# Kernel optimization log

Measured on AMD Instinct MI355X. Metric: run time of the kernel, lower is better.

The kernel has to match this reference:

```python
import jax, jax.numpy as jnp
import numpy as np

D_MODEL = 1024
D_FF = 2048
N_EXPERTS = 8
TOP_K = 2


def setup_inputs() -> dict:
    key = jax.random.key(0)
    ks = jax.random.split(key, 10)
    s = 0.02
    return {
        "x": jax.random.normal(ks[0], (2, 1024, D_MODEL), dtype=jnp.float32),
        "gate_w": jax.random.normal(ks[1], (N_EXPERTS, D_MODEL), dtype=jnp.float32) * s,
        "gate_b": jnp.zeros((N_EXPERTS,), jnp.float32),
        "Wg": jax.random.normal(ks[2], (N_EXPERTS, D_MODEL, D_FF), dtype=jnp.float32) * s,
        "bg": jnp.zeros((N_EXPERTS, D_FF), jnp.float32),
        "Wu": jax.random.normal(ks[3], (N_EXPERTS, D_MODEL, D_FF), dtype=jnp.float32) * s,
        "bu": jnp.zeros((N_EXPERTS, D_FF), jnp.float32),
        "Wd": jax.random.normal(ks[4], (N_EXPERTS, D_FF, D_MODEL), dtype=jnp.float32) * s,
        "bd": jnp.zeros((N_EXPERTS, D_MODEL), jnp.float32),
    }


def reference(x, gate_w, gate_b, Wg, bg, Wu, bu, Wd, bd):
    b, s, d = x.shape
    xf = x.reshape(-1, d)                       # (T, d)
    T = xf.shape[0]
    # --- router ---
    logits = xf @ gate_w.T + gate_b             # (T, E)
    probs = jax.nn.softmax(logits.astype(jnp.float32), axis=-1)
    # load-balance loss: KL(ideal || mean_probs), reduction='sum'
    expert_probs = probs.mean(axis=0)
    ideal = 1.0 / N_EXPERTS
    balance_loss = jnp.sum(ideal * (jnp.log(ideal) - jnp.log(expert_probs + 1e-9)))
    # top-k routing, renormalized
    vals, idx = jax.lax.top_k(probs, TOP_K)     # (T, K)
    w = vals / vals.sum(axis=-1, keepdims=True)
    # per-token per-expert combine weight (T, E); zero for non-selected experts
    cw = jnp.zeros((T, N_EXPERTS), jnp.float32).at[
        jnp.arange(T)[:, None], idx].add(w)
    # --- experts (SwiGLU MLP), batched over E, masked combine ---
    g = jnp.einsum('td,edf->tef', xf, Wg) + bg[None]   # (T, E, F)
    u = jnp.einsum('td,edf->tef', xf, Wu) + bu[None]
    h = jax.nn.silu(g) * u
    out = jnp.einsum('tef,efd->ted', h, Wd) + bd[None]  # (T, E, d)
    y = jnp.einsum('ted,te->td', out, cw.astype(x.dtype))
    return y.reshape(b, s, d), balance_loss
```

## Files before the change

### kernel.cpp

```cpp
#include <hip/hip_runtime.h>
#include <hip/hip_bf16.h>


#define D_MODEL 1024
#define D_FF    2048
#define N_EXP   8
#define T_TOK   2048
#define MAXTILES 40

typedef __attribute__((ext_vector_type(8))) short bf16x8;
typedef __attribute__((ext_vector_type(8))) ushort u16x8;
typedef __attribute__((ext_vector_type(4))) float f32x4;

__device__ __forceinline__ ushort f2bf(float f) {
    union { float f; unsigned u; } c; c.f = f;
    unsigned u = c.u;
    return (ushort)((u + 0x7fffu + ((u >> 16) & 1u)) >> 16);
}

__device__ __forceinline__ void glds16(const void* g, void* l) {
    __builtin_amdgcn_global_load_lds(
        (const __attribute__((address_space(1))) unsigned int*)g,
        (__attribute__((address_space(3))) unsigned int*)l, 16, 0, 0);
}

__device__ __forceinline__ void prep_slab_gwu(
    int sp, int tid, const float* __restrict__ Wg, const float* __restrict__ Wu,
    ushort* __restrict__ Wgt, ushort* __restrict__ Wut, ushort* lds)
{
    int which = sp >> 10, s = sp & 1023;
    const float* src = which ? Wu : Wg;
    ushort* dst = which ? Wut : Wgt;
    int e = s >> 7, kt = (s >> 3) & 15, kb = s & 7;
    const float4* p = (const float4*)(src + (size_t)e * 1024 * 2048 + (size_t)(kt * 64 + kb * 8) * 2048);
#pragma unroll
    for (int i = 0; i < 16; i++) {
        float4 v = p[i * 256 + tid];
        ushort4 o;
        o.x = f2bf(v.x); o.y = f2bf(v.y); o.z = f2bf(v.z); o.w = f2bf(v.w);
        *(ushort4*)&lds[(i * 256 + tid) * 4] = o;
    }
    __syncthreads();
    u16x8 in[8];
#pragma unroll
    for (int ko = 0; ko < 8; ko++)
        in[ko] = *(const u16x8*)&lds[ko * 2048 + tid * 8];
    u16x8 out[8];
#pragma unroll
    for (int j = 0; j < 8; j++)
#pragma unroll
        for (int ko = 0; ko < 8; ko++)
            out[j][ko] = in[ko][j];
    __syncthreads();
    int swz = (tid & 7) << 4;
#pragma unroll
    for (int j = 0; j < 8; j++)
        *(u16x8*)((char*)lds + (((8 * tid + j) * 16) ^ swz)) = out[j];
    __syncthreads();
#pragma unroll
    for (int i = 0; i < 8; i++) {
        int c = i * 256 + tid;
        u16x8 v = *(const u16x8*)((char*)lds + ((c * 16) ^ (((c >> 3) & 7) << 4)));
        int R = c >> 7, q = c & 127;
        *(u16x8*)&dst[(size_t)(e * 256 + R * 16 + kt) * 8192 + kb * 1024 + q * 8] = v;
    }
}

__device__ __forceinline__ void prep_slab_wd(
    int s, int tid, const float* __restrict__ Wd, ushort* __restrict__ Wdt, ushort* lds)
{
    int e = s >> 7, kt = (s >> 2) & 31, kbp = s & 3;
    const float4* p = (const float4*)(Wd + (size_t)e * 2048 * 1024 + (size_t)(kt * 64 + kbp * 16) * 1024);
#pragma unroll
    for (int i = 0; i < 16; i++) {
        float4 v = p[i * 256 + tid];
        ushort4 o;
        o.x = f2bf(v.x); o.y = f2bf(v.y); o.z = f2bf(v.z); o.w = f2bf(v.w);
        *(ushort4*)&lds[(i * 256 + tid) * 4] = o;
    }
    __syncthreads();
    u16x8 in[8];
    int th = tid >> 7, tc = tid & 127;
#pragma unroll
    for (int ko = 0; ko < 8; ko++)
        in[ko] = *(const u16x8*)&lds[(th * 8 + ko) * 1024 + tc * 8];
    u16x8 out[8];
#pragma unroll
    for (int j = 0; j < 8; j++)
#pragma unroll
        for (int ko = 0; ko < 8; ko++)
            out[j][ko] = in[ko][j];
    __syncthreads();
    int swz = (tid & 7) << 4;
#pragma unroll
    for (int j = 0; j < 8; j++)
        *(u16x8*)((char*)lds + (((8 * tid + j) * 16) ^ swz)) = out[j];
    __syncthreads();
#pragma unroll
    for (int i = 0; i < 8; i++) {
        int c = i * 256 + tid;
        u16x8 v = *(const u16x8*)((char*)lds + ((c * 16) ^ (((c >> 3) & 7) << 4)));
        int R = c >> 7, q = c & 127;
        int kb2 = R >> 3, ntp = R & 7;
        *(u16x8*)&Wdt[(size_t)(e * 256 + ntp * 32 + kt) * 8192 + (kbp * 2 + kb2) * 1024 + q * 8] = v;
    }
}

union SM1 {
    float gws[N_EXP * D_MODEL];
    ushort prep[16384];
};

__global__ __launch_bounds__(256) void k_router_prep(
    const float* __restrict__ x, const float* __restrict__ gw, const float* __restrict__ gb,
    int* cnt, float* probsum, int* tok, int* slotpk, float* wtok,
    ushort* __restrict__ xb,
    const float* __restrict__ Wg, const float* __restrict__ Wu,
    ushort* __restrict__ Wgt, ushort* __restrict__ Wut)
{
    __shared__ __align__(16) SM1 sm;
    __shared__ float ps_s[N_EXP];
    __shared__ int   bc_s[N_EXP];
    __shared__ int   gb_s[N_EXP];
    __shared__ int   a_e[64];
    __shared__ int   a_lp[64];

    int tid = threadIdx.x;
    int bid = blockIdx.x;

    if (bid >= 64) {
        prep_slab_gwu(bid - 64, tid, Wg, Wu, Wgt, Wut, sm.prep);
        return;
    }

    float* gws = sm.gws;
    for (int i = tid; i < N_EXP * D_MODEL / 4; i += 256)
        ((float4*)gws)[i] = ((const float4*)gw)[i];
    if (tid < N_EXP) { ps_s[tid] = 0.f; bc_s[tid] = 0; }
    __syncthreads();

    int wave = tid >> 6, lane = tid & 63;

    for (int it = 0; it < 8; it++) {
        int tb = it * 4 + wave;
        int t = bid * 32 + tb;
        const float4* xr = (const float4*)(x + (size_t)t * D_MODEL);
        ushort* xbr = xb + (size_t)t * D_MODEL;

        float acc[N_EXP];
#pragma unroll
        for (int e = 0; e < N_EXP; e++) acc[e] = 0.f;
#pragma unroll
        for (int q = 0; q < 4; q++) {
            int idx = q * 64 + lane;
            float4 xv = xr[idx];
            ushort4 xc;
            xc.x = f2bf(xv.x); xc.y = f2bf(xv.y); xc.z = f2bf(xv.z); xc.w = f2bf(xv.w);
            *(ushort4*)&xbr[idx * 4] = xc;
#pragma unroll
            for (int e = 0; e < N_EXP; e++) {
                float4 gv = ((const float4*)(gws + e * D_MODEL))[idx];
                acc[e] += xv.x * gv.x + xv.y * gv.y + xv.z * gv.z + xv.w * gv.w;
            }
        }
#pragma unroll
        for (int off = 32; off > 0; off >>= 1) {
#pragma unroll
            for (int e = 0; e < N_EXP; e++) acc[e] += __shfl_xor(acc[e], off, 64);
        }
        if (lane == 0) {
            float l[N_EXP], m = -1e30f;
#pragma unroll
            for (int e = 0; e < N_EXP; e++) { l[e] = acc[e] + gb[e]; m = fmaxf(m, l[e]); }
            float p[N_EXP], s = 0.f;
#pragma unroll
            for (int e = 0; e < N_EXP; e++) { p[e] = expf(l[e] - m); s += p[e]; }
            float inv = 1.f / s;
#pragma unroll
            for (int e = 0; e < N_EXP; e++) { p[e] *= inv; atomicAdd(&ps_s[e], p[e]); }
            int i0 = 0; float v0 = p[0];
#pragma unroll
            for (int e = 1; e < N_EXP; e++) if (p[e] > v0) { v0 = p[e]; i0 = e; }
            int i1 = -1; float v1 = -1.f;
#pragma unroll
            for (int e = 0; e < N_EXP; e++) if (e != i0 && p[e] > v1) { v1 = p[e]; i1 = e; }
            float winv = 1.f / (v0 + v1);
            int lp0 = atomicAdd(&bc_s[i0], 1);
            int lp1 = atomicAdd(&bc_s[i1], 1);
            a_e[tb * 2 + 0] = i0; a_lp[tb * 2 + 0] = lp0;
            a_e[tb * 2 + 1] = i1; a_lp[tb * 2 + 1] = lp1;
            wtok[t * 2 + 0] = v0 * winv;
            wtok[t * 2 + 1] = v1 * winv;
        }
    }
    __syncthreads();
    if (tid < N_EXP) {
        gb_s[tid] = atomicAdd(&cnt[tid], bc_s[tid]);
        atomicAdd(&probsum[tid], ps_s[tid]);
    }
    __syncthreads();
    if (tid < 64) {
        int tb = tid >> 1, k = tid & 1;
        int t = bid * 32 + tb;
        int e = a_e[tid];
        int slot = gb_s[e] + a_lp[tid];
        tok[e * T_TOK + slot] = t;
        slotpk[t * 2 + k] = (e << 16) | slot;
    }
}

__global__ void k_base_loss(const int* __restrict__ cnt, const float* __restrict__ probsum,
                            int* abase, int* tile, float* loss_out)
{
    if (threadIdx.x == 0 && blockIdx.x == 0) {
        int b = 0, nt = 0;
        float loss = 0.f;
        for (int e = 0; e < N_EXP; e++) {
            abase[e] = b;
            for (int m0 = 0; m0 < cnt[e]; m0 += 128)
                tile[nt++] = (e << 16) | m0;
            b += ((cnt[e] + 127) >> 7) * 128;
            float mean = probsum[e] * (1.0f / T_TOK);
            loss += 0.125f * (logf(0.125f) - logf(mean + 1e-9f));
        }
        for (; nt < MAXTILES; nt++) tile[nt] = -1;
        *loss_out = loss;
    }
}

struct SM_GU { ushort As[128 * 88]; ushort Bg[8192]; ushort Bu[8192]; };
union SM3 {
    SM_GU g;
    ushort prep[16384];
};

__global__ __launch_bounds__(256, 2) void k_gu_prepwd(
    const ushort* __restrict__ Wgt, const ushort* __restrict__ Wut,
    const float* __restrict__ bg, const float* __restrict__ bu,
    const ushort* __restrict__ xb, const int* __restrict__ cnt,
    const int* __restrict__ abase, const int* __restrict__ tile,
    const int* __restrict__ tok, ushort* __restrict__ h_t,
    const float* __restrict__ Wd, ushort* __restrict__ Wdt)
{
    __shared__ __align__(16) SM3 sm;

    int bid = blockIdx.x;
    int tid = threadIdx.x;

    if (bid >= MAXTILES * 16) {
        prep_slab_wd(bid - MAXTILES * 16, tid, Wd, Wdt, sm.prep);
        return;
    }

    int ti = tile[bid % MAXTILES];
    if (ti < 0) return;
    int e = ti >> 16, m0 = ti & 0xffff;
    int ne = cnt[e];
    int nt = bid / MAXTILES;
    int n0 = nt * 128;
    int stile = (abase[e] >> 7) + (m0 >> 7);

    ushort* As = sm.g.As;
    ushort* Bg_s = sm.g.Bg;
    ushort* Bu_s = sm.g.Bu;

    int lane = tid & 63, wave = tid >> 6;
    int wm = (wave & 1) * 64, wn = (wave >> 1) * 64;

    int arow = tid >> 1;
    int akh = (tid & 1) * 32;
    int atok = tok[e * T_TOK + min(m0 + arow, ne - 1)];
    const ushort* xrow = xb + (size_t)atok * D_MODEL;

    const char* gbase = (const char*)(Wgt + (size_t)(e * 16 + nt) * 16 * 8192);
    const char* ubase = (const char*)(Wut + (size_t)(e * 16 + nt) * 16 * 8192);
    int goff = tid * 16;
    int loff = (tid >> 6) * 1024;

    f32x4 accg[4][4], accu[4][4];
#pragma unroll
    for (int i = 0; i < 4; i++)
#pragma unroll
        for (int j = 0; j < 4; j++) {
            accg[i][j] = (f32x4){0.f, 0.f, 0.f, 0.f};
            accu[i][j] = (f32x4){0.f, 0.f, 0.f, 0.f};
        }

    for (int kt = 0; kt < D_MODEL / 64; kt++) {
        __syncthreads();
#pragma unroll
        for (int q = 0; q < 4; q++)
            *(uint4*)&As[arow * 88 + akh + q * 8] = *(const uint4*)&xrow[kt * 64 + akh + q * 8];
        const char* gsrc = gbase + kt * 16384;
        const char* usrc = ubase + kt * 16384;
#pragma unroll
        for (int q = 0; q < 4; q++) {
            glds16(gsrc + q * 4096 + goff, (char*)Bg_s + q * 4096 + loff);
            glds16(usrc + q * 4096 + goff, (char*)Bu_s + q * 4096 + loff);
        }
        __syncthreads();
#pragma unroll
        for (int ks = 0; ks < 2; ks++) {
            bf16x8 af[4];
            int arow_f = wm + (lane & 15);
            int akb = ks * 32 + (lane >> 4) * 8;
#pragma unroll
            for (int sm_ = 0; sm_ < 4; sm_++)
                af[sm_] = *(const bf16x8*)&As[(arow_f + sm_ * 16) * 88 + akb];
            int bkb = ks * 4 + (lane >> 4);
#pragma unroll
            for (int sn = 0; sn < 4; sn++) {
                int ncol = wn + sn * 16 + (lane & 15);
                bf16x8 bgf = *(const bf16x8*)&Bg_s[(bkb * 128 + ncol) * 8];
                bf16x8 buf = *(const bf16x8*)&Bu_s[(bkb * 128 + ncol) * 8];
#pragma unroll
                for (int sm_ = 0; sm_ < 4; sm_++) {
                    accg[sm_][sn] = __builtin_amdgcn_mfma_f32_16x16x32_bf16(af[sm_], bgf, accg[sm_][sn], 0, 0, 0);
                    accu[sm_][sn] = __builtin_amdgcn_mfma_f32_16x16x32_bf16(af[sm_], buf, accu[sm_][sn], 0, 0, 0);
                }
            }
        }
    }
    int rbase = wm + ((lane >> 4) << 2);
    int cbase = wn + (lane & 15);
    size_t tbase = (size_t)stile * 32 * 8192;
#pragma unroll
    for (int sm_ = 0; sm_ < 4; sm_++) {
#pragma unroll
        for (int r = 0; r < 4; r++) {
            int pos = m0 + rbase + sm_ * 16 + r;
            if (pos < ne) {
                int row = pos & 127;
#pragma unroll
                for (int sn = 0; sn < 4; sn++) {
                    int col = n0 + cbase + sn * 16;
                    float g = accg[sm_][sn][r] + bg[e * D_FF + col];
                    float u = accu[sm_][sn][r] + bu[e * D_FF + col];
                    float hv = (g / (1.f + expf(-g))) * u;
                    int ktb = col >> 6, kb = (col >> 3) & 7, ko = col & 7;
                    h_t[tbase + (size_t)ktb * 8192 + (kb * 128 + row) * 8 + ko] = f2bf(hv);
                }
            }
        }
    }
}

__global__ __launch_bounds__(256, 2) void k_expert_down(
    const ushort* __restrict__ Wdt, const float* __restrict__ bd,
    const ushort* __restrict__ h_t, const int* __restrict__ cnt,
    const int* __restrict__ abase, const int* __restrict__ tile,
    float* __restrict__ outp)
{
    int ti = tile[blockIdx.x];
    if (ti < 0) return;
    int e = ti >> 16, m0 = ti & 0xffff;
    int ne = cnt[e];
    int nt = blockIdx.y;
    int n0 = nt * 128;
    int stile = (abase[e] >> 7) + (m0 >> 7);

    __shared__ __align__(16) ushort As8[8192];
    __shared__ __align__(16) ushort Bd_s[8192];

    int tid = threadIdx.x;
    int lane = tid & 63, wave = tid >> 6;
    int wm = (wave & 1) * 64, wn = (wave >> 1) * 64;

    const char* hbase = (const char*)(h_t + (size_t)stile * 32 * 8192);
    const char* dbase = (const char*)(Wdt + (size_t)(e * 8 + nt) * 32 * 8192);
    int goff = tid * 16;
    int loff = (tid >> 6) * 1024;

    f32x4 acc[4][4];
#pragma unroll
    for (int i = 0; i < 4; i++)
#pragma unroll
        for (int j = 0; j < 4; j++) acc[i][j] = (f32x4){0.f, 0.f, 0.f, 0.f};

    for (int kt = 0; kt < D_FF / 64; kt++) {
        __syncthreads();
        const char* asrc = hbase + kt * 16384;
        const char* bsrc = dbase + kt * 16384;
#pragma unroll
        for (int q = 0; q < 4; q++) {
            glds16(asrc + q * 4096 + goff, (char*)As8 + q * 4096 + loff);
            glds16(bsrc + q * 4096 + goff, (char*)Bd_s + q * 4096 + loff);
        }
        __syncthreads();
#pragma unroll
        for (int ks = 0; ks < 2; ks++) {
            bf16x8 af[4];
            int kb = ks * 4 + (lane >> 4);
            int arow_f = wm + (lane & 15);
#pragma unroll
            for (int sm_ = 0; sm_ < 4; sm_++)
                af[sm_] = *(const bf16x8*)&As8[(kb * 128 + arow_f + sm_ * 16) * 8];
#pragma unroll
            for (int sn = 0; sn < 4; sn++) {
                int ncol = wn + sn * 16 + (lane & 15);
                bf16x8 bdf = *(const bf16x8*)&Bd_s[(kb * 128 + ncol) * 8];
#pragma unroll
                for (int sm_ = 0; sm_ < 4; sm_++)
                    acc[sm_][sn] = __builtin_amdgcn_mfma_f32_16x16x32_bf16(af[sm_], bdf, acc[sm_][sn], 0, 0, 0);
            }
        }
    }
    int rbase = wm + ((lane >> 4) << 2);
    int cbase = wn + (lane & 15);
#pragma unroll
    for (int sm_ = 0; sm_ < 4; sm_++) {
#pragma unroll
        for (int r = 0; r < 4; r++) {
            int pos = m0 + rbase + sm_ * 16 + r;
            if (pos < ne) {
                size_t ob = (size_t)(abase[e] + pos) * D_MODEL;
#pragma unroll
                for (int sn = 0; sn < 4; sn++) {
                    int col = n0 + cbase + sn * 16;
                    outp[ob + col] = acc[sm_][sn][r] + bd[e * D_MODEL + col];
                }
            }
        }
    }
}

__global__ void k_combine(const float* __restrict__ outp, const int* __restrict__ slotpk,
                          const float* __restrict__ wtok, const int* __restrict__ abase,
                          float* __restrict__ y)
{
    int idx = blockIdx.x * 256 + threadIdx.x;
    int t = idx >> 8, j = idx & 255;
    int sp0 = slotpk[t * 2 + 0], sp1 = slotpk[t * 2 + 1];
    float w0 = wtok[t * 2 + 0], w1 = wtok[t * 2 + 1];
    size_t s0 = (size_t)abase[sp0 >> 16] + (sp0 & 0xffff);
    size_t s1 = (size_t)abase[sp1 >> 16] + (sp1 & 0xffff);
    float4 a = ((const float4*)outp)[s0 * (D_MODEL / 4) + j];
    float4 b = ((const float4*)outp)[s1 * (D_MODEL / 4) + j];
    float4 o;
    o.x = w0 * a.x + w1 * b.x;
    o.y = w0 * a.y + w1 * b.y;
    o.z = w0 * a.z + w1 * b.z;
    o.w = w0 * a.w + w1 * b.w;
    ((float4*)y)[idx] = o;
}

extern "C" void kernel_launch(void* const* d_in, const int* in_sizes, int n_in,
                              void* d_out, int out_size, void* d_ws, size_t ws_size,
                              hipStream_t stream)
{
    const float* x  = (const float*)d_in[0];
    const float* gw = (const float*)d_in[1];
    const float* gb = (const float*)d_in[2];
    const float* Wg = (const float*)d_in[3];
    const float* bg = (const float*)d_in[4];
    const float* Wu = (const float*)d_in[5];
    const float* bu = (const float*)d_in[6];
    const float* Wd = (const float*)d_in[7];
    const float* bd = (const float*)d_in[8];
    float* y = (float*)d_out;
    float* loss_out = y + (size_t)T_TOK * D_MODEL;

    char* ws = (char*)d_ws;
    int*    cnt     = (int*)(ws + 0);
    float*  probsum = (float*)(ws + 128);
    int*    abase   = (int*)(ws + 256);
    int*    tiletab = (int*)(ws + 320);
    int*    slotpk  = (int*)(ws + 512);
    float*  wtok    = (float*)(ws + 16896);
    int*    tok     = (int*)(ws + 33280);
    ushort* xb      = (ushort*)(ws + 131072);
    ushort* Wgt     = (ushort*)(ws + 4325376);
    ushort* Wut     = (ushort*)(ws + 37879808);
    ushort* Wdt     = (ushort*)(ws + 71434240);
    ushort* h_t     = (ushort*)(ws + 104988672);
    float*  outp    = (float*)(ws + 125960192);

    (void)hipMemsetAsync(d_ws, 0, 256, stream);
    k_router_prep<<<dim3(64 + 2048), dim3(256), 0, stream>>>(
        x, gw, gb, cnt, probsum, tok, slotpk, wtok, xb, Wg, Wu, Wgt, Wut);
    k_base_loss<<<dim3(1), dim3(64), 0, stream>>>(cnt, probsum, abase, tiletab, loss_out);
    k_gu_prepwd<<<dim3(MAXTILES * 16 + 1024), dim3(256), 0, stream>>>(
        Wgt, Wut, bg, bu, xb, cnt, abase, tiletab, tok, h_t, Wd, Wdt);
    k_expert_down<<<dim3(MAXTILES, 8), dim3(256), 0, stream>>>(Wdt, bd, h_t, cnt, abase, tiletab, outp);
    k_combine<<<dim3(2048), dim3(256), 0, stream>>>(outp, slotpk, wtok, abase, y);
}
```

Baseline: 349.0 us.

## Fuse combine into down-projection epilogue via atomic adds; shrink A-tile stride

Removes the separate combine kernel and the fp32 per-slot expert output buffer. The down-projection epilogue now scales each row by its per-slot routing weight and atomically adds it into y, which is zeroed with a memset first. The gate/up kernel's LDS A-tile stride drops from 88 to 72, and its launch bounds ask for 3 blocks per CU. This trades an extra kernel launch and a round trip through global memory for float atomics plus a memset, and the new stride may change LDS bank conflicts.

```diff
diff --git a/kernel.cpp b/kernel.cpp
--- a/kernel.cpp
+++ b/kernel.cpp
@@ -7,6 +7,7 @@
 #define N_EXP   8
 #define T_TOK   2048
 #define MAXTILES 40
+#define ASTRIDE 72
 
 typedef __attribute__((ext_vector_type(8))) short bf16x8;
 typedef __attribute__((ext_vector_type(8))) ushort u16x8;
@@ -113,7 +114,7 @@
 
 __global__ __launch_bounds__(256) void k_router_prep(
     const float* __restrict__ x, const float* __restrict__ gw, const float* __restrict__ gb,
-    int* cnt, float* probsum, int* tok, int* slotpk, float* wtok,
+    int* cnt, float* probsum, int* tok, float* wslot,
     ushort* __restrict__ xb,
     const float* __restrict__ Wg, const float* __restrict__ Wu,
     ushort* __restrict__ Wgt, ushort* __restrict__ Wut)
@@ -124,6 +125,7 @@
     __shared__ int   gb_s[N_EXP];
     __shared__ int   a_e[64];
     __shared__ int   a_lp[64];
+    __shared__ float a_w[64];
 
     int tid = threadIdx.x;
     int bid = blockIdx.x;
@@ -187,10 +189,8 @@
             float winv = 1.f / (v0 + v1);
             int lp0 = atomicAdd(&bc_s[i0], 1);
             int lp1 = atomicAdd(&bc_s[i1], 1);
-            a_e[tb * 2 + 0] = i0; a_lp[tb * 2 + 0] = lp0;
-            a_e[tb * 2 + 1] = i1; a_lp[tb * 2 + 1] = lp1;
-            wtok[t * 2 + 0] = v0 * winv;
-            wtok[t * 2 + 1] = v1 * winv;
+            a_e[tb * 2 + 0] = i0; a_lp[tb * 2 + 0] = lp0; a_w[tb * 2 + 0] = v0 * winv;
+            a_e[tb * 2 + 1] = i1; a_lp[tb * 2 + 1] = lp1; a_w[tb * 2 + 1] = v1 * winv;
         }
     }
     __syncthreads();
@@ -200,12 +200,12 @@
     }
     __syncthreads();
     if (tid < 64) {
-        int tb = tid >> 1, k = tid & 1;
+        int tb = tid >> 1;
         int t = bid * 32 + tb;
         int e = a_e[tid];
         int slot = gb_s[e] + a_lp[tid];
         tok[e * T_TOK + slot] = t;
-        slotpk[t * 2 + k] = (e << 16) | slot;
+        wslot[e * T_TOK + slot] = a_w[tid];
     }
 }
 
@@ -228,13 +228,13 @@
     }
 }
 
-struct SM_GU { ushort As[128 * 88]; ushort Bg[8192]; ushort Bu[8192]; };
+struct SM_GU { ushort As[128 * ASTRIDE]; ushort Bg[8192]; ushort Bu[8192]; };
 union SM3 {
     SM_GU g;
     ushort prep[16384];
 };
 
-__global__ __launch_bounds__(256, 2) void k_gu_prepwd(
+__global__ __launch_bounds__(256, 3) void k_gu_prepwd(
     const ushort* __restrict__ Wgt, const ushort* __restrict__ Wut,
     const float* __restrict__ bg, const float* __restrict__ bu,
     const ushort* __restrict__ xb, const int* __restrict__ cnt,
@@ -290,7 +290,7 @@
         __syncthreads();
 #pragma unroll
         for (int q = 0; q < 4; q++)
-            *(uint4*)&As[arow * 88 + akh + q * 8] = *(const uint4*)&xrow[kt * 64 + akh + q * 8];
+            *(uint4*)&As[arow * ASTRIDE + akh + q * 8] = *(const uint4*)&xrow[kt * 64 + akh + q * 8];
         const char* gsrc = gbase + kt * 16384;
         const char* usrc = ubase + kt * 16384;
 #pragma unroll
@@ -306,7 +306,7 @@
             int akb = ks * 32 + (lane >> 4) * 8;
 #pragma unroll
             for (int sm_ = 0; sm_ < 4; sm_++)
-                af[sm_] = *(const bf16x8*)&As[(arow_f + sm_ * 16) * 88 + akb];
+                af[sm_] = *(const bf16x8*)&As[(arow_f + sm_ * 16) * ASTRIDE + akb];
             int bkb = ks * 4 + (lane >> 4);
 #pragma unroll
             for (int sn = 0; sn < 4; sn++) {
@@ -345,11 +345,12 @@
     }
 }
 
-__global__ __launch_bounds__(256, 2) void k_expert_down(
+__global__ __launch_bounds__(256, 2) void k_down_combine(
     const ushort* __restrict__ Wdt, const float* __restrict__ bd,
     const ushort* __restrict__ h_t, const int* __restrict__ cnt,
     const int* __restrict__ abase, const int* __restrict__ tile,
-    float* __restrict__ outp)
+    const int* __restrict__ tok, const float* __restrict__ wslot,
+    float* __restrict__ y)
 {
     int ti = tile[blockIdx.x];
     if (ti < 0) return;
@@ -413,35 +414,17 @@
         for (int r = 0; r < 4; r++) {
             int pos = m0 + rbase + sm_ * 16 + r;
             if (pos < ne) {
-                size_t ob = (size_t)(abase[e] + pos) * D_MODEL;
+                int t = tok[e * T_TOK + pos];
+                float w = wslot[e * T_TOK + pos];
+                float* yrow = y + (size_t)t * D_MODEL;
 #pragma unroll
                 for (int sn = 0; sn < 4; sn++) {
                     int col = n0 + cbase + sn * 16;
-                    outp[ob + col] = acc[sm_][sn][r] + bd[e * D_MODEL + col];
+                    atomicAdd(&yrow[col], w * (acc[sm_][sn][r] + bd[e * D_MODEL + col]));
                 }
             }
         }
     }
-}
-
-__global__ void k_combine(const float* __restrict__ outp, const int* __restrict__ slotpk,
-                          const float* __restrict__ wtok, const int* __restrict__ abase,
-                          float* __restrict__ y)
-{
-    int idx = blockIdx.x * 256 + threadIdx.x;
-    int t = idx >> 8, j = idx & 255;
-    int sp0 = slotpk[t * 2 + 0], sp1 = slotpk[t * 2 + 1];
-    float w0 = wtok[t * 2 + 0], w1 = wtok[t * 2 + 1];
-    size_t s0 = (size_t)abase[sp0 >> 16] + (sp0 & 0xffff);
-    size_t s1 = (size_t)abase[sp1 >> 16] + (sp1 & 0xffff);
-    float4 a = ((const float4*)outp)[s0 * (D_MODEL / 4) + j];
-    float4 b = ((const float4*)outp)[s1 * (D_MODEL / 4) + j];
-    float4 o;
-    o.x = w0 * a.x + w1 * b.x;
-    o.y = w0 * a.y + w1 * b.y;
-    o.z = w0 * a.z + w1 * b.z;
-    o.w = w0 * a.w + w1 * b.w;
-    ((float4*)y)[idx] = o;
 }
 
 extern "C" void kernel_launch(void* const* d_in, const int* in_sizes, int n_in,
@@ -465,22 +448,21 @@
     float*  probsum = (float*)(ws + 128);
     int*    abase   = (int*)(ws + 256);
     int*    tiletab = (int*)(ws + 320);
-    int*    slotpk  = (int*)(ws + 512);
-    float*  wtok    = (float*)(ws + 16896);
-    int*    tok     = (int*)(ws + 33280);
-    ushort* xb      = (ushort*)(ws + 131072);
-    ushort* Wgt     = (ushort*)(ws + 4325376);
-    ushort* Wut     = (ushort*)(ws + 37879808);
-    ushort* Wdt     = (ushort*)(ws + 71434240);
-    ushort* h_t     = (ushort*)(ws + 104988672);
-    float*  outp    = (float*)(ws + 125960192);
+    float*  wslot   = (float*)(ws + 1024);
+    int*    tok     = (int*)(ws + 66560);
+    ushort* xb      = (ushort*)(ws + 135168);
+    ushort* Wgt     = (ushort*)(ws + 4329472);
+    ushort* Wut     = (ushort*)(ws + 37883904);
+    ushort* Wdt     = (ushort*)(ws + 71438336);
+    ushort* h_t     = (ushort*)(ws + 104992768);
 
     (void)hipMemsetAsync(d_ws, 0, 256, stream);
+    (void)hipMemsetAsync(y, 0, (size_t)T_TOK * D_MODEL * sizeof(float), stream);
     k_router_prep<<<dim3(64 + 2048), dim3(256), 0, stream>>>(
-        x, gw, gb, cnt, probsum, tok, slotpk, wtok, xb, Wg, Wu, Wgt, Wut);
+        x, gw, gb, cnt, probsum, tok, wslot, xb, Wg, Wu, Wgt, Wut);
     k_base_loss<<<dim3(1), dim3(64), 0, stream>>>(cnt, probsum, abase, tiletab, loss_out);
     k_gu_prepwd<<<dim3(MAXTILES * 16 + 1024), dim3(256), 0, stream>>>(
         Wgt, Wut, bg, bu, xb, cnt, abase, tiletab, tok, h_t, Wd, Wdt);
-    k_expert_down<<<dim3(MAXTILES, 8), dim3(256), 0, stream>>>(Wdt, bd, h_t, cnt, abase, tiletab, outp);
-    k_combine<<<dim3(2048), dim3(256), 0, stream>>>(outp, slotpk, wtok, abase, y);
-}
+    k_down_combine<<<dim3(MAXTILES, 8), dim3(256), 0, stream>>>(
+        Wdt, bd, h_t, cnt, abase, tiletab, tok, wslot, y);
+}
```

New measurement: 379.1 us. +8.6%, slower.

## Double-buffer weight tiles and load activation fragments directly from global

Applied to the files above, without the earlier changes.

Both expert GEMM kernels now keep two LDS buffers for the weight tiles and prefetch the next k-tile while MFMAs run on the current one, leaving one barrier per step instead of two. The activation (A) operand no longer goes through shared memory; each lane reads its MFMA fragments directly from global memory into registers, prefetching the next tile. This is meant to hide load latency and cut LDS traffic and barriers. In exchange it uses more registers and relies on cache for the scattered, per-lane gathered activation reads, which may be less coalesced.

```diff
diff --git a/kernel.cpp b/kernel.cpp
--- a/kernel.cpp
+++ b/kernel.cpp
@@ -118,7 +118,7 @@
     const float* __restrict__ Wg, const float* __restrict__ Wu,
     ushort* __restrict__ Wgt, ushort* __restrict__ Wut)
 {
-    __shared__ __align__(16) SM1 sm;
+    __shared__ __align__(16) SM1 smem;
     __shared__ float ps_s[N_EXP];
     __shared__ int   bc_s[N_EXP];
     __shared__ int   gb_s[N_EXP];
@@ -129,11 +129,11 @@
     int bid = blockIdx.x;
 
     if (bid >= 64) {
-        prep_slab_gwu(bid - 64, tid, Wg, Wu, Wgt, Wut, sm.prep);
+        prep_slab_gwu(bid - 64, tid, Wg, Wu, Wgt, Wut, smem.prep);
         return;
     }
 
-    float* gws = sm.gws;
+    float* gws = smem.gws;
     for (int i = tid; i < N_EXP * D_MODEL / 4; i += 256)
         ((float4*)gws)[i] = ((const float4*)gw)[i];
     if (tid < N_EXP) { ps_s[tid] = 0.f; bc_s[tid] = 0; }
@@ -228,7 +228,7 @@
     }
 }
 
-struct SM_GU { ushort As[128 * 88]; ushort Bg[8192]; ushort Bu[8192]; };
+struct SM_GU { ushort Bg[2][8192]; ushort Bu[2][8192]; };
 union SM3 {
     SM_GU g;
     ushort prep[16384];
@@ -242,13 +242,13 @@
     const int* __restrict__ tok, ushort* __restrict__ h_t,
     const float* __restrict__ Wd, ushort* __restrict__ Wdt)
 {
-    __shared__ __align__(16) SM3 sm;
+    __shared__ __align__(16) SM3 smem;
 
     int bid = blockIdx.x;
     int tid = threadIdx.x;
 
     if (bid >= MAXTILES * 16) {
-        prep_slab_wd(bid - MAXTILES * 16, tid, Wd, Wdt, sm.prep);
+        prep_slab_wd(bid - MAXTILES * 16, tid, Wd, Wdt, smem.prep);
         return;
     }
 
@@ -260,23 +260,25 @@
     int n0 = nt * 128;
     int stile = (abase[e] >> 7) + (m0 >> 7);
 
-    ushort* As = sm.g.As;
-    ushort* Bg_s = sm.g.Bg;
-    ushort* Bu_s = sm.g.Bu;
-
     int lane = tid & 63, wave = tid >> 6;
     int wm = (wave & 1) * 64, wn = (wave >> 1) * 64;
 
-    int arow = tid >> 1;
-    int akh = (tid & 1) * 32;
-    int atok = tok[e * T_TOK + min(m0 + arow, ne - 1)];
-    const ushort* xrow = xb + (size_t)atok * D_MODEL;
+    const ushort* arowp[4];
+#pragma unroll
+    for (int s_ = 0; s_ < 4; s_++) {
+        int pos = min(m0 + wm + (lane & 15) + s_ * 16, ne - 1);
+        arowp[s_] = xb + (size_t)tok[e * T_TOK + pos] * D_MODEL;
+    }
+    int klo = (lane >> 4) * 8;
 
     const char* gbase = (const char*)(Wgt + (size_t)(e * 16 + nt) * 16 * 8192);
     const char* ubase = (const char*)(Wut + (size_t)(e * 16 + nt) * 16 * 8192);
     int goff = tid * 16;
     int loff = (tid >> 6) * 1024;
 
+    ushort* Bg0 = smem.g.Bg[0]; ushort* Bg1 = smem.g.Bg[1];
+    ushort* Bu0 = smem.g.Bu[0]; ushort* Bu1 = smem.g.Bu[1];
+
     f32x4 accg[4][4], accu[4][4];
 #pragma unroll
     for (int i = 0; i < 4; i++)
@@ -286,41 +288,67 @@
             accu[i][j] = (f32x4){0.f, 0.f, 0.f, 0.f};
         }
 
-    for (int kt = 0; kt < D_MODEL / 64; kt++) {
+    bf16x8 afA[4], afB[4];
+#pragma unroll
+    for (int s_ = 0; s_ < 4; s_++)
+        afA[s_] = *(const bf16x8*)(arowp[s_] + klo);
+#pragma unroll
+    for (int q = 0; q < 4; q++) {
+        glds16(gbase + q * 4096 + goff, (char*)Bg0 + q * 4096 + loff);
+        glds16(ubase + q * 4096 + goff, (char*)Bu0 + q * 4096 + loff);
+    }
+    __syncthreads();
+
+    auto STEP = [&](int kt, bf16x8 (&afc)[4], bf16x8 (&afn)[4],
+                    ushort* Bgc, ushort* Buc, ushort* Bgn, ushort* Bun) {
+        bf16x8 af1[4];
+#pragma unroll
+        for (int s_ = 0; s_ < 4; s_++)
+            af1[s_] = *(const bf16x8*)(arowp[s_] + kt * 64 + 32 + klo);
+        if (kt < 15) {
+#pragma unroll
+            for (int s_ = 0; s_ < 4; s_++)
+                afn[s_] = *(const bf16x8*)(arowp[s_] + (kt + 1) * 64 + klo);
+            const char* gsrc = gbase + (kt + 1) * 16384;
+            const char* usrc = ubase + (kt + 1) * 16384;
+#pragma unroll
+            for (int q = 0; q < 4; q++) {
+                glds16(gsrc + q * 4096 + goff, (char*)Bgn + q * 4096 + loff);
+                glds16(usrc + q * 4096 + goff, (char*)Bun + q * 4096 + loff);
+            }
+        }
+#pragma unroll
+        for (int sn = 0; sn < 4; sn++) {
+            int ncol = wn + sn * 16 + (lane & 15);
+            int bkb = lane >> 4;
+            bf16x8 bgf = *(const bf16x8*)&Bgc[(bkb * 128 + ncol) * 8];
+            bf16x8 buf_ = *(const bf16x8*)&Buc[(bkb * 128 + ncol) * 8];
+#pragma unroll
+            for (int s_ = 0; s_ < 4; s_++) {
+                accg[s_][sn] = __builtin_amdgcn_mfma_f32_16x16x32_bf16(afc[s_], bgf, accg[s_][sn], 0, 0, 0);
+                accu[s_][sn] = __builtin_amdgcn_mfma_f32_16x16x32_bf16(afc[s_], buf_, accu[s_][sn], 0, 0, 0);
+            }
+        }
+#pragma unroll
+        for (int sn = 0; sn < 4; sn++) {
+            int ncol = wn + sn * 16 + (lane & 15);
+            int bkb = 4 + (lane >> 4);
+            bf16x8 bgf = *(const bf16x8*)&Bgc[(bkb * 128 + ncol) * 8];
+            bf16x8 buf_ = *(const bf16x8*)&Buc[(bkb * 128 + ncol) * 8];
+#pragma unroll
+            for (int s_ = 0; s_ < 4; s_++) {
+                accg[s_][sn] = __builtin_amdgcn_mfma_f32_16x16x32_bf16(af1[s_], bgf, accg[s_][sn], 0, 0, 0);
+                accu[s_][sn] = __builtin_amdgcn_mfma_f32_16x16x32_bf16(af1[s_], buf_, accu[s_][sn], 0, 0, 0);
+            }
+        }
         __syncthreads();
-#pragma unroll
-        for (int q = 0; q < 4; q++)
-            *(uint4*)&As[arow * 88 + akh + q * 8] = *(const uint4*)&xrow[kt * 64 + akh + q * 8];
-        const char* gsrc = gbase + kt * 16384;
-        const char* usrc = ubase + kt * 16384;
-#pragma unroll
-        for (int q = 0; q < 4; q++) {
-            glds16(gsrc + q * 4096 + goff, (char*)Bg_s + q * 4096 + loff);
-            glds16(usrc + q * 4096 + goff, (char*)Bu_s + q * 4096 + loff);
-        }
-        __syncthreads();
-#pragma unroll
-        for (int ks = 0; ks < 2; ks++) {
-            bf16x8 af[4];
-            int arow_f = wm + (lane & 15);
-            int akb = ks * 32 + (lane >> 4) * 8;
-#pragma unroll
-            for (int sm_ = 0; sm_ < 4; sm_++)
-                af[sm_] = *(const bf16x8*)&As[(arow_f + sm_ * 16) * 88 + akb];
-            int bkb = ks * 4 + (lane >> 4);
-#pragma unroll
-            for (int sn = 0; sn < 4; sn++) {
-                int ncol = wn + sn * 16 + (lane & 15);
-                bf16x8 bgf = *(const bf16x8*)&Bg_s[(bkb * 128 + ncol) * 8];
-                bf16x8 buf = *(const bf16x8*)&Bu_s[(bkb * 128 + ncol) * 8];
-#pragma unroll
-                for (int sm_ = 0; sm_ < 4; sm_++) {
-                    accg[sm_][sn] = __builtin_amdgcn_mfma_f32_16x16x32_bf16(af[sm_], bgf, accg[sm_][sn], 0, 0, 0);
-                    accu[sm_][sn] = __builtin_amdgcn_mfma_f32_16x16x32_bf16(af[sm_], buf, accu[sm_][sn], 0, 0, 0);
-                }
-            }
-        }
-    }
+    };
+
+    for (int kt = 0; kt < 16; kt += 2) {
+        STEP(kt,     afA, afB, Bg0, Bu0, Bg1, Bu1);
+        STEP(kt + 1, afB, afA, Bg1, Bu1, Bg0, Bu0);
+    }
+
     int rbase = wm + ((lane >> 4) << 2);
     int cbase = wn + (lane & 15);
     size_t tbase = (size_t)stile * 32 * 8192;
@@ -359,8 +387,7 @@
     int n0 = nt * 128;
     int stile = (abase[e] >> 7) + (m0 >> 7);
 
-    __shared__ __align__(16) ushort As8[8192];
-    __shared__ __align__(16) ushort Bd_s[8192];
+    __shared__ __align__(16) ushort Bd_s[2][8192];
 
     int tid = threadIdx.x;
     int lane = tid & 63, wave = tid >> 6;
@@ -371,40 +398,72 @@
     int goff = tid * 16;
     int loff = (tid >> 6) * 1024;
 
+    int arow_f = wm + (lane & 15);
+    int a0off[4], a1off[4];
+#pragma unroll
+    for (int s_ = 0; s_ < 4; s_++) {
+        a0off[s_] = ((lane >> 4) * 128 + arow_f + s_ * 16) * 16;
+        a1off[s_] = ((4 + (lane >> 4)) * 128 + arow_f + s_ * 16) * 16;
+    }
+
+    ushort* Bd0 = Bd_s[0]; ushort* Bd1 = Bd_s[1];
+
     f32x4 acc[4][4];
 #pragma unroll
     for (int i = 0; i < 4; i++)
 #pragma unroll
         for (int j = 0; j < 4; j++) acc[i][j] = (f32x4){0.f, 0.f, 0.f, 0.f};
 
-    for (int kt = 0; kt < D_FF / 64; kt++) {
+    bf16x8 afA[4], afB[4];
+#pragma unroll
+    for (int s_ = 0; s_ < 4; s_++)
+        afA[s_] = *(const bf16x8*)(hbase + a0off[s_]);
+#pragma unroll
+    for (int q = 0; q < 4; q++)
+        glds16(dbase + q * 4096 + goff, (char*)Bd0 + q * 4096 + loff);
+    __syncthreads();
+
+    auto STEP = [&](int kt, bf16x8 (&afc)[4], bf16x8 (&afn)[4],
+                    ushort* Bdc, ushort* Bdn) {
+        bf16x8 af1[4];
+#pragma unroll
+        for (int s_ = 0; s_ < 4; s_++)
+            af1[s_] = *(const bf16x8*)(hbase + kt * 16384 + a1off[s_]);
+        if (kt < 31) {
+#pragma unroll
+            for (int s_ = 0; s_ < 4; s_++)
+                afn[s_] = *(const bf16x8*)(hbase + (kt + 1) * 16384 + a0off[s_]);
+            const char* bsrc = dbase + (kt + 1) * 16384;
+#pragma unroll
+            for (int q = 0; q < 4; q++)
+                glds16(bsrc + q * 4096 + goff, (char*)Bdn + q * 4096 + loff);
+        }
+#pragma unroll
+        for (int sn = 0; sn < 4; sn++) {
+            int ncol = wn + sn * 16 + (lane & 15);
+            int bkb = lane >> 4;
+            bf16x8 bdf = *(const bf16x8*)&Bdc[(bkb * 128 + ncol) * 8];
+#pragma unroll
+            for (int s_ = 0; s_ < 4; s_++)
+                acc[s_][sn] = __builtin_amdgcn_mfma_f32_16x16x32_bf16(afc[s_], bdf, acc[s_][sn], 0, 0, 0);
+        }
+#pragma unroll
+        for (int sn = 0; sn < 4; sn++) {
+            int ncol = wn + sn * 16 + (lane & 15);
+            int bkb = 4 + (lane >> 4);
+            bf16x8 bdf = *(const bf16x8*)&Bdc[(bkb * 128 + ncol) * 8];
+#pragma unroll
+            for (int s_ = 0; s_ < 4; s_++)
+                acc[s_][sn] = __builtin_amdgcn_mfma_f32_16x16x32_bf16(af1[s_], bdf, acc[s_][sn], 0, 0, 0);
+        }
         __syncthreads();
-        const char* asrc = hbase + kt * 16384;
-        const char* bsrc = dbase + kt * 16384;
-#pragma unroll
-        for (int q = 0; q < 4; q++) {
-            glds16(asrc + q * 4096 + goff, (char*)As8 + q * 4096 + loff);
-            glds16(bsrc + q * 4096 + goff, (char*)Bd_s + q * 4096 + loff);
-        }
-        __syncthreads();
-#pragma unroll
-        for (int ks = 0; ks < 2; ks++) {
-            bf16x8 af[4];
-            int kb = ks * 4 + (lane >> 4);
-            int arow_f = wm + (lane & 15);
-#pragma unroll
-            for (int sm_ = 0; sm_ < 4; sm_++)
-                af[sm_] = *(const bf16x8*)&As8[(kb * 128 + arow_f + sm_ * 16) * 8];
-#pragma unroll
-            for (int sn = 0; sn < 4; sn++) {
-                int ncol = wn + sn * 16 + (lane & 15);
-                bf16x8 bdf = *(const bf16x8*)&Bd_s[(kb * 128 + ncol) * 8];
-#pragma unroll
-                for (int sm_ = 0; sm_ < 4; sm_++)
-                    acc[sm_][sn] = __builtin_amdgcn_mfma_f32_16x16x32_bf16(af[sm_], bdf, acc[sm_][sn], 0, 0, 0);
-            }
-        }
-    }
+    };
+
+    for (int kt = 0; kt < 32; kt += 2) {
+        STEP(kt,     afA, afB, Bd0, Bd1);
+        STEP(kt + 1, afB, afA, Bd1, Bd0);
+    }
+
     int rbase = wm + ((lane >> 4) << 2);
     int cbase = wn + (lane & 15);
 #pragma unroll
@@ -481,6 +540,7 @@
     k_base_loss<<<dim3(1), dim3(64), 0, stream>>>(cnt, probsum, abase, tiletab, loss_out);
     k_gu_prepwd<<<dim3(MAXTILES * 16 + 1024), dim3(256), 0, stream>>>(
         Wgt, Wut, bg, bu, xb, cnt, abase, tiletab, tok, h_t, Wd, Wdt);
-    k_expert_down<<<dim3(MAXTILES, 8), dim3(256), 0, stream>>>(Wdt, bd, h_t, cnt, abase, tiletab, outp);
+    k_expert_down<<<dim3(MAXTILES, 8), dim3(256), 0, stream>>>(
+        Wdt, bd, h_t, cnt, abase, tiletab, outp);
     k_combine<<<dim3(2048), dim3(256), 0, stream>>>(outp, slotpk, wtok, abase, y);
 }
```

New measurement: 425.3 us. 21.9% more time.

## Fuse Wd bf16 conversion into down-proj GEMM with register-prefetched loads

Applied to the files above, without the earlier changes.

Removes the separate Wd fp32-to-bf16 pre-transpose pass that ran as extra blocks of the gate/up kernel, and instead has the down-projection kernel read fp32 Wd directly, convert to bf16 in registers and store it into shared memory in the MFMA layout. The h tiles and Wd rows for the next k-step are prefetched into registers before the current step's MFMAs, replacing the async global-to-LDS loads. This avoids writing and re-reading the bf16 Wd copy. In exchange, each down-proj tile reads fp32 Wd (twice the bytes) and converts it redundantly across the token tiles of the same expert, and register pressure rises.

```diff
diff --git a/kernel.cpp b/kernel.cpp
--- a/kernel.cpp
+++ b/kernel.cpp
@@ -63,46 +63,6 @@
         u16x8 v = *(const u16x8*)((char*)lds + ((c * 16) ^ (((c >> 3) & 7) << 4)));
         int R = c >> 7, q = c & 127;
         *(u16x8*)&dst[(size_t)(e * 256 + R * 16 + kt) * 8192 + kb * 1024 + q * 8] = v;
-    }
-}
-
-__device__ __forceinline__ void prep_slab_wd(
-    int s, int tid, const float* __restrict__ Wd, ushort* __restrict__ Wdt, ushort* lds)
-{
-    int e = s >> 7, kt = (s >> 2) & 31, kbp = s & 3;
-    const float4* p = (const float4*)(Wd + (size_t)e * 2048 * 1024 + (size_t)(kt * 64 + kbp * 16) * 1024);
-#pragma unroll
-    for (int i = 0; i < 16; i++) {
-        float4 v = p[i * 256 + tid];
-        ushort4 o;
-        o.x = f2bf(v.x); o.y = f2bf(v.y); o.z = f2bf(v.z); o.w = f2bf(v.w);
-        *(ushort4*)&lds[(i * 256 + tid) * 4] = o;
-    }
-    __syncthreads();
-    u16x8 in[8];
-    int th = tid >> 7, tc = tid & 127;
-#pragma unroll
-    for (int ko = 0; ko < 8; ko++)
-        in[ko] = *(const u16x8*)&lds[(th * 8 + ko) * 1024 + tc * 8];
-    u16x8 out[8];
-#pragma unroll
-    for (int j = 0; j < 8; j++)
-#pragma unroll
-        for (int ko = 0; ko < 8; ko++)
-            out[j][ko] = in[ko][j];
-    __syncthreads();
-    int swz = (tid & 7) << 4;
-#pragma unroll
-    for (int j = 0; j < 8; j++)
-        *(u16x8*)((char*)lds + (((8 * tid + j) * 16) ^ swz)) = out[j];
-    __syncthreads();
-#pragma unroll
-    for (int i = 0; i < 8; i++) {
-        int c = i * 256 + tid;
-        u16x8 v = *(const u16x8*)((char*)lds + ((c * 16) ^ (((c >> 3) & 7) << 4)));
-        int R = c >> 7, q = c & 127;
-        int kb2 = R >> 3, ntp = R & 7;
-        *(u16x8*)&Wdt[(size_t)(e * 256 + ntp * 32 + kt) * 8192 + (kbp * 2 + kb2) * 1024 + q * 8] = v;
     }
 }
 
@@ -118,7 +78,7 @@
     const float* __restrict__ Wg, const float* __restrict__ Wu,
     ushort* __restrict__ Wgt, ushort* __restrict__ Wut)
 {
-    __shared__ __align__(16) SM1 sm;
+    __shared__ __align__(16) SM1 smem;
     __shared__ float ps_s[N_EXP];
     __shared__ int   bc_s[N_EXP];
     __shared__ int   gb_s[N_EXP];
@@ -129,11 +89,11 @@
     int bid = blockIdx.x;
 
     if (bid >= 64) {
-        prep_slab_gwu(bid - 64, tid, Wg, Wu, Wgt, Wut, sm.prep);
+        prep_slab_gwu(bid - 64, tid, Wg, Wu, Wgt, Wut, smem.prep);
         return;
     }
 
-    float* gws = sm.gws;
+    float* gws = smem.gws;
     for (int i = tid; i < N_EXP * D_MODEL / 4; i += 256)
         ((float4*)gws)[i] = ((const float4*)gw)[i];
     if (tid < N_EXP) { ps_s[tid] = 0.f; bc_s[tid] = 0; }
@@ -228,42 +188,26 @@
     }
 }
 
-struct SM_GU { ushort As[128 * 88]; ushort Bg[8192]; ushort Bu[8192]; };
-union SM3 {
-    SM_GU g;
-    ushort prep[16384];
-};
-
-__global__ __launch_bounds__(256, 2) void k_gu_prepwd(
+__global__ __launch_bounds__(256, 2) void k_expert_gu(
     const ushort* __restrict__ Wgt, const ushort* __restrict__ Wut,
     const float* __restrict__ bg, const float* __restrict__ bu,
     const ushort* __restrict__ xb, const int* __restrict__ cnt,
     const int* __restrict__ abase, const int* __restrict__ tile,
-    const int* __restrict__ tok, ushort* __restrict__ h_t,
-    const float* __restrict__ Wd, ushort* __restrict__ Wdt)
-{
-    __shared__ __align__(16) SM3 sm;
-
-    int bid = blockIdx.x;
-    int tid = threadIdx.x;
-
-    if (bid >= MAXTILES * 16) {
-        prep_slab_wd(bid - MAXTILES * 16, tid, Wd, Wdt, sm.prep);
-        return;
-    }
-
-    int ti = tile[bid % MAXTILES];
+    const int* __restrict__ tok, ushort* __restrict__ h_t)
+{
+    int ti = tile[blockIdx.x];
     if (ti < 0) return;
     int e = ti >> 16, m0 = ti & 0xffff;
     int ne = cnt[e];
-    int nt = bid / MAXTILES;
+    int nt = blockIdx.y;
     int n0 = nt * 128;
     int stile = (abase[e] >> 7) + (m0 >> 7);
 
-    ushort* As = sm.g.As;
-    ushort* Bg_s = sm.g.Bg;
-    ushort* Bu_s = sm.g.Bu;
-
+    __shared__ __align__(16) ushort As[128 * 88];
+    __shared__ __align__(16) ushort Bg_s[8192];
+    __shared__ __align__(16) ushort Bu_s[8192];
+
+    int tid = threadIdx.x;
     int lane = tid & 63, wave = tid >> 6;
     int wm = (wave & 1) * 64, wn = (wave >> 1) * 64;
 
@@ -346,7 +290,7 @@
 }
 
 __global__ __launch_bounds__(256, 2) void k_expert_down(
-    const ushort* __restrict__ Wdt, const float* __restrict__ bd,
+    const float* __restrict__ Wd, const float* __restrict__ bd,
     const ushort* __restrict__ h_t, const int* __restrict__ cnt,
     const int* __restrict__ abase, const int* __restrict__ tile,
     float* __restrict__ outp)
@@ -366,25 +310,43 @@
     int lane = tid & 63, wave = tid >> 6;
     int wm = (wave & 1) * 64, wn = (wave >> 1) * 64;
 
-    const char* hbase = (const char*)(h_t + (size_t)stile * 32 * 8192);
-    const char* dbase = (const char*)(Wdt + (size_t)(e * 8 + nt) * 32 * 8192);
-    int goff = tid * 16;
-    int loff = (tid >> 6) * 1024;
+    const uint4* hbase = (const uint4*)(h_t + (size_t)stile * 32 * 8192);
+
+    int skb = tid >> 5, sc4 = (tid & 31) * 4;
+    const float* dp = Wd + (size_t)e * D_FF * D_MODEL + (size_t)(skb * 8) * D_MODEL + n0 + sc4;
+    ushort* dds = Bd_s + (skb * 128 + sc4) * 8;
 
     f32x4 acc[4][4];
 #pragma unroll
     for (int i = 0; i < 4; i++)
 #pragma unroll
         for (int j = 0; j < 4; j++) acc[i][j] = (f32x4){0.f, 0.f, 0.f, 0.f};
+
+    uint4 va[4];
+    float4 vd[8];
+#pragma unroll
+    for (int q = 0; q < 4; q++) va[q] = hbase[q * 256 + tid];
+#pragma unroll
+    for (int j = 0; j < 8; j++) vd[j] = *(const float4*)(dp + (size_t)j * D_MODEL);
 
     for (int kt = 0; kt < D_FF / 64; kt++) {
         __syncthreads();
-        const char* asrc = hbase + kt * 16384;
-        const char* bsrc = dbase + kt * 16384;
-#pragma unroll
-        for (int q = 0; q < 4; q++) {
-            glds16(asrc + q * 4096 + goff, (char*)As8 + q * 4096 + loff);
-            glds16(bsrc + q * 4096 + goff, (char*)Bd_s + q * 4096 + loff);
+#pragma unroll
+        for (int q = 0; q < 4; q++) ((uint4*)As8)[q * 256 + tid] = va[q];
+        u16x8 d0, d1, d2, d3;
+#pragma unroll
+        for (int j = 0; j < 8; j++) {
+            d0[j] = f2bf(vd[j].x); d1[j] = f2bf(vd[j].y); d2[j] = f2bf(vd[j].z); d3[j] = f2bf(vd[j].w);
+        }
+        *(u16x8*)(dds + 0)  = d0; *(u16x8*)(dds + 8)  = d1;
+        *(u16x8*)(dds + 16) = d2; *(u16x8*)(dds + 24) = d3;
+        if (kt < D_FF / 64 - 1) {
+            const uint4* hn = hbase + (kt + 1) * 1024;
+            const float* dn = dp + (size_t)(kt + 1) * 64 * D_MODEL;
+#pragma unroll
+            for (int q = 0; q < 4; q++) va[q] = hn[q * 256 + tid];
+#pragma unroll
+            for (int j = 0; j < 8; j++) vd[j] = *(const float4*)(dn + (size_t)j * D_MODEL);
         }
         __syncthreads();
 #pragma unroll
@@ -471,16 +433,16 @@
     ushort* xb      = (ushort*)(ws + 131072);
     ushort* Wgt     = (ushort*)(ws + 4325376);
     ushort* Wut     = (ushort*)(ws + 37879808);
-    ushort* Wdt     = (ushort*)(ws + 71434240);
-    ushort* h_t     = (ushort*)(ws + 104988672);
-    float*  outp    = (float*)(ws + 125960192);
+    ushort* h_t     = (ushort*)(ws + 71434240);
+    float*  outp    = (float*)(ws + 92405760);
 
     (void)hipMemsetAsync(d_ws, 0, 256, stream);
     k_router_prep<<<dim3(64 + 2048), dim3(256), 0, stream>>>(
         x, gw, gb, cnt, probsum, tok, slotpk, wtok, xb, Wg, Wu, Wgt, Wut);
     k_base_loss<<<dim3(1), dim3(64), 0, stream>>>(cnt, probsum, abase, tiletab, loss_out);
-    k_gu_prepwd<<<dim3(MAXTILES * 16 + 1024), dim3(256), 0, stream>>>(
-        Wgt, Wut, bg, bu, xb, cnt, abase, tiletab, tok, h_t, Wd, Wdt);
-    k_expert_down<<<dim3(MAXTILES, 8), dim3(256), 0, stream>>>(Wdt, bd, h_t, cnt, abase, tiletab, outp);
+    k_expert_gu<<<dim3(MAXTILES, 16), dim3(256), 0, stream>>>(
+        Wgt, Wut, bg, bu, xb, cnt, abase, tiletab, tok, h_t);
+    k_expert_down<<<dim3(MAXTILES, 8), dim3(256), 0, stream>>>(
+        Wd, bd, h_t, cnt, abase, tiletab, outp);
     k_combine<<<dim3(2048), dim3(256), 0, stream>>>(outp, slotpk, wtok, abase, y);
 }
```

Result: slower. 401.1 us (+14.9%).
